# Kernel tuning notes

Hardware: AMD Instinct MI355X
Metric: run time of the kernel (lower is better)

## Reference

```python
import jax, jax.numpy as jnp
import numpy as np

B, N, IN, HID, OUT = 32, 128, 64, 128, 64
_off = np.ones((N, N)) - np.eye(N)
RECV, SEND = np.where(_off)  # rel_rec one-hot rows -> receiver idx, rel_send -> sender idx
E = N * (N - 1)


def _bn(x, g, b):
    # BatchNorm1d in training mode over flattened (B*M, C), eps=1e-5, biased var
    c = x.shape[-1]
    xf = x.reshape(-1, c)
    m = xf.mean(0)
    v = ((xf - m) ** 2).mean(0)
    return (((xf - m) / jnp.sqrt(v + 1e-5)) * g + b).reshape(x.shape)


def _mlp(x, W1, b1, W2, b2, g, b):
    h = jax.nn.silu(x @ W1 + b1)
    h = jax.nn.silu(h @ W2 + b2)
    return _bn(h, g, b)


def setup_inputs() -> dict:
    key = jax.random.key(0)
    ks = jax.random.split(key, 8)
    p = lambda k, s: jax.random.normal(k, s, dtype=jnp.float32) * 0.05
    return {
        "node_feature": jax.random.normal(ks[0], (B, N, IN), dtype=jnp.float32),
        "nodes_mask": jnp.ones((B, N), dtype=jnp.float32),
        "edges_mask": jnp.ones((B, E), dtype=jnp.float32),
        "eW1": p(ks[1], (2 * IN, HID)), "eb1": jnp.full((HID,), 0.1, jnp.float32),
        "eW2": p(ks[2], (HID, HID)), "eb2": jnp.full((HID,), 0.1, jnp.float32),
        "eg": jnp.ones((HID,), jnp.float32), "ebt": jnp.zeros((HID,), jnp.float32),
        "nW1": p(ks[3], (HID, HID)), "nb1": jnp.full((HID,), 0.1, jnp.float32),
        "nW2": p(ks[4], (HID, HID)), "nb2": jnp.full((HID,), 0.1, jnp.float32),
        "ng": jnp.ones((HID,), jnp.float32), "nbt": jnp.zeros((HID,), jnp.float32),
        "mW1": p(ks[5], (IN + HID, HID)), "mb1": jnp.full((HID,), 0.1, jnp.float32),
        "mW2": p(ks[6], (HID, OUT)), "mb2": jnp.full((OUT,), 0.1, jnp.float32),
        "mg": jnp.ones((OUT,), jnp.float32), "mbt": jnp.zeros((OUT,), jnp.float32),
        "t_nodes": 0, "t_edges": 0,
    }


def reference(node_feature, nodes_mask, edges_mask,
              eW1, eb1, eW2, eb2, eg, ebt,
              nW1, nb1, nW2, nb2, ng, nbt,
              mW1, mb1, mW2, mb2, mg, mbt,
              t_nodes, t_edges):
    # edge_model: rel_send/rel_rec one-hot matmuls == gathers
    senders = node_feature[:, SEND, :]    # [B,E,IN]
    receivers = node_feature[:, RECV, :]  # [B,E,IN]
    ef = jnp.concatenate([senders, receivers], axis=-1)  # [B,E,2*IN]
    # skip_first_edge_type=True, edge_types=2 -> only edge_nn[1], norm=1.0
    em = edges_mask[:, :, None]
    msg = _mlp(ef, eW1, eb1, eW2, eb2, eg, ebt) * em  # [B,E,HID]
    mij = msg / 1.0
    out = mij * em       # attention=False
    mij_m = mij * em
    # node_model: rel_rec.T matmul == scatter-sum over receivers, then / N
    incoming = jnp.zeros((B, N, HID), msg.dtype).at[:, RECV, :].add(out) / N
    incoming = _mlp(incoming, nW1, nb1, nW2, nb2, ng, nbt) * nodes_mask[:, :, None]
    nef = jnp.concatenate([node_feature, incoming], axis=-1)  # [B,N,IN+HID]
    out_node = _mlp(nef, mW1, mb1, mW2, mb2, mg, mbt) * nodes_mask[:, :, None]
    return (out_node, mij_m)
```

## Files before the change

kernel.cpp:

```cpp
#include <hip/hip_runtime.h>
#include <hip/hip_bf16.h>

#define BB    32
#define NNODE 128
#define INF   64
#define HIDF  128
#define OUTF  64
#define EE    (NNODE*(NNODE-1))
#define TILES 127
#define NBLK_EDGE (BB*TILES)
#define ROWS_E 520192.0f
#define ROWS_N 4096.0f
#define OUT0_ELEMS (BB*NNODE*OUTF)
#define H2_ELEMS ((size_t)520192*128)

typedef __bf16 bf16_t;
typedef __bf16 bfrag8 __attribute__((ext_vector_type(8)));
typedef float  floatx4 __attribute__((ext_vector_type(4)));

__device__ __forceinline__ float ld_g(const void* p, size_t i, int bf) {
    return bf ? (float)((const bf16_t*)p)[i] : ((const float*)p)[i];
}
__device__ __forceinline__ void st_g(void* p, size_t i, float v, int bf) {
    if (bf) ((bf16_t*)p)[i] = (bf16_t)v; else ((float*)p)[i] = v;
}
__device__ __forceinline__ void* mij_ptr(void* dout, int bf) {
    return bf ? (void*)((bf16_t*)dout + OUT0_ELEMS)
              : (void*)((float*)dout + OUT0_ELEMS);
}
__device__ __forceinline__ float silu_f(float x) {
    return x * __builtin_amdgcn_rcpf(1.0f + __expf(-x));
}

__device__ __forceinline__ int swz_col(int row, int col)  {
    return col ^ ((row & 15) << 3);
}
__device__ __forceinline__ int swz64_col(int row, int col) {
    return col ^ ((row & 7) << 3);
}

__global__ __launch_bounds__(256)
void k_prep(const unsigned int* __restrict__ eg_words,
            const void* __restrict__ W1g, const void* __restrict__ W2g,
            bf16_t* __restrict__ Wf1, bf16_t* __restrict__ Wf2,
            int* __restrict__ flag, float* __restrict__ totE)
{
    const int bf = (eg_words[0] == 0x3F803F80u) ? 1 : 0;
    if (blockIdx.x == 0) {
        if (threadIdx.x == 0) *flag = bf;
        totE[threadIdx.x] = 0.f;
    }
    const int idx = blockIdx.x*256 + threadIdx.x;
    const int mat = idx >> 14;
    const int e   = idx & 16383;
    const int n   = e & 127, k = e >> 7;
    const float v = ld_g(mat ? W2g : W1g, e, bf);
    const int NB = n >> 4, ln = n & 15;
    const int ks = k >> 5, q = (k >> 3) & 3, j = k & 7;
    bf16_t* dst = mat ? Wf2 : Wf1;
    dst[((((NB*4 + ks)*4 + q)*16 + ln) << 3) + j] = (bf16_t)v;
}

__global__ __launch_bounds__(256)
void k_sr(const void* __restrict__ nf,
          const bf16_t* __restrict__ Wf1, const void* __restrict__ b1g,
          float* __restrict__ Sbuf, float* __restrict__ Rbuf,
          const int* __restrict__ flagp)
{
    __shared__ __align__(16) bf16_t lA[128*64];
    const int bf  = *flagp;
    const int r0  = blockIdx.x * 128;
    const int tid = threadIdx.x;

#pragma unroll
    for (int s = 0; s < 4; ++s) {
        const int u = tid + s*256;
        const int m = u >> 3;
        const int c = (u & 7) ^ (m & 7);
        const size_t gi = (size_t)(r0 + m)*INF + c*8;
        if (bf) {
            ((uint4*)lA)[u] = *(const uint4*)((const bf16_t*)nf + gi);
        } else {
            const float4 f0 = *(const float4*)((const float*)nf + gi);
            const float4 f1 = *(const float4*)((const float*)nf + gi + 4);
            bfrag8 v;
            v[0]=(bf16_t)f0.x; v[1]=(bf16_t)f0.y; v[2]=(bf16_t)f0.z; v[3]=(bf16_t)f0.w;
            v[4]=(bf16_t)f1.x; v[5]=(bf16_t)f1.y; v[6]=(bf16_t)f1.z; v[7]=(bf16_t)f1.w;
            *(bfrag8*)(lA + (size_t)u*8) = v;
        }
    }
    __syncthreads();

    const int w  = tid >> 6;
    const int L  = tid & 63;
    const int wr = w >> 1;
    const int wc = w & 1;
    const int q  = L >> 4;
    const int ln = L & 15;

    const floatx4 zero4 = {0.f, 0.f, 0.f, 0.f};
    floatx4 accS[4][4], accR[4][4];
#pragma unroll
    for (int mt = 0; mt < 4; ++mt)
#pragma unroll
        for (int nt = 0; nt < 4; ++nt) { accS[mt][nt] = zero4; accR[mt][nt] = zero4; }

#pragma unroll
    for (int ks = 0; ks < 2; ++ks) {
        bfrag8 af[4], bs[4], br[4];
#pragma unroll
        for (int mt = 0; mt < 4; ++mt) {
            const int Rr = wr*64 + mt*16 + ln;
            af[mt] = *(const bfrag8*)(lA + Rr*64 + swz64_col(Rr, ks*32 + q*8));
        }
#pragma unroll
        for (int nt = 0; nt < 4; ++nt) {
            bs[nt] = *(const bfrag8*)(Wf1 + ((size_t)((wc*4 + nt)*4 + ks)*64 + L)*8);
            br[nt] = *(const bfrag8*)(Wf1 + ((size_t)((wc*4 + nt)*4 + ks + 2)*64 + L)*8);
        }
#pragma unroll
        for (int mt = 0; mt < 4; ++mt)
#pragma unroll
            for (int nt = 0; nt < 4; ++nt) {
                accS[mt][nt] = __builtin_amdgcn_mfma_f32_16x16x32_bf16(
                    af[mt], bs[nt], accS[mt][nt], 0, 0, 0);
                accR[mt][nt] = __builtin_amdgcn_mfma_f32_16x16x32_bf16(
                    af[mt], br[nt], accR[mt][nt], 0, 0, 0);
            }
    }

#pragma unroll
    for (int nt = 0; nt < 4; ++nt) {
        const int col = wc*64 + nt*16 + ln;
        const float bias = ld_g(b1g, col, bf);
#pragma unroll
        for (int mt = 0; mt < 4; ++mt)
#pragma unroll
            for (int r = 0; r < 4; ++r) {
                const int row = wr*64 + mt*16 + q*4 + r;
                Sbuf[(size_t)(r0 + row)*128 + col] = accS[mt][nt][r] + bias;
                Rbuf[(size_t)(r0 + row)*128 + col] = accR[mt][nt][r];
            }
    }
}

__global__ __launch_bounds__(256, 4)
void k_edge_mlp(const float* __restrict__ Sbuf, const float* __restrict__ Rbuf,
                const bf16_t* __restrict__ Wf2, const void* __restrict__ b2g,
                void* __restrict__ dout, bf16_t* __restrict__ h2ws,
                const int* __restrict__ flagp, float* __restrict__ totE,
                int h2mode)
{
    __shared__ __align__(16) bf16_t lA[128*128];
    __shared__ float sSum[128], sQ[128];
    const int bf  = *flagp;
    void* h2out = mij_ptr(dout, bf);
    const int bx   = blockIdx.x;
    const int bIdx = bx / TILES;
    const int t    = bx - bIdx*TILES;
    const int tid  = threadIdx.x;

    if (tid < 128) { sSum[tid] = 0.f; sQ[tid] = 0.f; }

    {
        const size_t nodeBase = (size_t)bIdx*NNODE*128;
#pragma unroll
        for (int s = 0; s < 8; ++s) {
            const int u = tid + s*256;
            const int m = u >> 4;
            const int c = (u & 15) ^ (m & 15);
            const int eb = t*128 + m;
            const unsigned recv = ((unsigned)eb * 33027u) >> 22;
            const unsigned rr   = (unsigned)eb - recv*127u;
            const unsigned send = rr + (rr >= recv ? 1u : 0u);
            const float* Sp = Sbuf + nodeBase + (size_t)send*128 + c*8;
            const float* Rp = Rbuf + nodeBase + (size_t)recv*128 + c*8;
            const float4 s0 = *(const float4*)Sp;
            const float4 s1 = *(const float4*)(Sp + 4);
            const float4 r0v = *(const float4*)Rp;
            const float4 r1v = *(const float4*)(Rp + 4);
            bfrag8 v;
            v[0]=(bf16_t)silu_f(s0.x + r0v.x); v[1]=(bf16_t)silu_f(s0.y + r0v.y);
            v[2]=(bf16_t)silu_f(s0.z + r0v.z); v[3]=(bf16_t)silu_f(s0.w + r0v.w);
            v[4]=(bf16_t)silu_f(s1.x + r1v.x); v[5]=(bf16_t)silu_f(s1.y + r1v.y);
            v[6]=(bf16_t)silu_f(s1.z + r1v.z); v[7]=(bf16_t)silu_f(s1.w + r1v.w);
            *(bfrag8*)(lA + (size_t)u*8) = v;
        }
    }
    __syncthreads();

    const int w  = tid >> 6;
    const int L  = tid & 63;
    const int wr = w >> 1;
    const int wc = w & 1;
    const int q  = L >> 4;
    const int ln = L & 15;

    const floatx4 zero4 = {0.f, 0.f, 0.f, 0.f};
    floatx4 acc[4][4];
#pragma unroll
    for (int mt = 0; mt < 4; ++mt)
#pragma unroll
        for (int nt = 0; nt < 4; ++nt) acc[mt][nt] = zero4;

#pragma unroll
    for (int ks = 0; ks < 4; ++ks) {
        const int kk = ks*32;
        bfrag8 af[4], bv[4];
#pragma unroll
        for (int mt = 0; mt < 4; ++mt) {
            const int R = wr*64 + mt*16 + ln;
            af[mt] = *(const bfrag8*)(lA + R*128 + swz_col(R, kk + q*8));
        }
#pragma unroll
        for (int nt = 0; nt < 4; ++nt)
            bv[nt] = *(const bfrag8*)(Wf2 + ((size_t)((wc*4 + nt)*4 + ks)*64 + L)*8);
#pragma unroll
        for (int mt = 0; mt < 4; ++mt)
#pragma unroll
            for (int nt = 0; nt < 4; ++nt)
                acc[mt][nt] = __builtin_amdgcn_mfma_f32_16x16x32_bf16(
                    af[mt], bv[nt], acc[mt][nt], 0, 0, 0);
    }
    __syncthreads();

#pragma unroll
    for (int nt = 0; nt < 4; ++nt) {
        const int col = wc*64 + nt*16 + ln;
        const float bias = ld_g(b2g, col, bf);
        float cs = 0.f, cq = 0.f;
#pragma unroll
        for (int mt = 0; mt < 4; ++mt)
#pragma unroll
            for (int r = 0; r < 4; ++r) {
                const int R = wr*64 + mt*16 + q*4 + r;
                const float v = silu_f(acc[mt][nt][r] + bias);
                cs += v; cq += v*v;
                lA[R*128 + swz_col(R, col)] = (bf16_t)v;
            }
        cs += __shfl_xor(cs, 16); cs += __shfl_xor(cs, 32);
        cq += __shfl_xor(cq, 16); cq += __shfl_xor(cq, 32);
        if (L < 16) { atomicAdd(&sSum[col], cs); atomicAdd(&sQ[col], cq); }
    }
    __syncthreads();

    {
        const size_t Rbase = ((size_t)bIdx*EE + (size_t)t*128) * 128;
#pragma unroll
        for (int s = 0; s < 8; ++s) {
            const int u = tid + s*256;
            const int m = u >> 4;
            const int c = (u & 15) ^ (m & 15);
            const size_t go = Rbase + (size_t)m*128 + c*8;
            if (h2mode) {
                *(uint4*)(h2ws + go) = ((const uint4*)lA)[u];
            } else if (bf) {
                *(uint4*)((bf16_t*)h2out + go) = ((const uint4*)lA)[u];
            } else {
                const bfrag8 vv = *(const bfrag8*)(lA + (size_t)u*8);
                float4 f0, f1;
                f0.x=(float)vv[0]; f0.y=(float)vv[1]; f0.z=(float)vv[2]; f0.w=(float)vv[3];
                f1.x=(float)vv[4]; f1.y=(float)vv[5]; f1.z=(float)vv[6]; f1.w=(float)vv[7];
                *(float4*)((float*)h2out + go)     = f0;
                *(float4*)((float*)h2out + go + 4) = f1;
            }
        }
        if (tid < 128) {
            atomicAdd(&totE[tid],       sSum[tid]);
            atomicAdd(&totE[128 + tid], sQ[tid]);
        }
    }
}

__global__ __launch_bounds__(256)
void k_bn_scatter(void* __restrict__ dout,
                  const bf16_t* __restrict__ h2ws,
                  const void* __restrict__ emask,
                  const float* __restrict__ totE,
                  const void* __restrict__ g, const void* __restrict__ bt,
                  float* __restrict__ inc,
                  const int* __restrict__ flagp, int h2mode)
{
    const int bf = *flagp;
    void* mij = mij_ptr(dout, bf);
    const void* h2 = h2mode ? (const void*)h2ws : (const void*)mij;
    const int h2bf = h2mode | bf;
    const int bx = blockIdx.x;
    const int b  = bx >> 7, i = bx & 127;
    const int tid = threadIdx.x;
    const int cg = tid & 15, p = tid >> 4;
    const int c0 = cg*8;
    float al[8], be[8];
#pragma unroll
    for (int j = 0; j < 8; ++j) {
        const int c = c0 + j;
        const float mn = totE[c] * (1.0f/ROWS_E);
        float vr = totE[128 + c] * (1.0f/ROWS_E) - mn*mn;
        vr = fmaxf(vr, 0.f);
        al[j] = ld_g(g, c, bf) * rsqrtf(vr + 1e-5f);
        be[j] = ld_g(bt, c, bf) - mn*al[j];
    }
    const size_t seg = (size_t)b*EE + (size_t)i*127;
    float s[8];
#pragma unroll
    for (int j = 0; j < 8; ++j) s[j] = 0.f;
    for (int e = p; e < 127; e += 16) {
        const float em  = ld_g(emask, seg + e, bf);
        const float em2 = em*em;
        const size_t base = (seg + e)*128 + c0;
        float v[8];
        if (h2bf) {
            const bfrag8 u = *(const bfrag8*)((const bf16_t*)h2 + base);
#pragma unroll
            for (int j = 0; j < 8; ++j) v[j] = (float)u[j];
        } else {
            const float4 f0 = *(const float4*)((const float*)h2 + base);
            const float4 f1 = *(const float4*)((const float*)h2 + base + 4);
            v[0]=f0.x; v[1]=f0.y; v[2]=f0.z; v[3]=f0.w;
            v[4]=f1.x; v[5]=f1.y; v[6]=f1.z; v[7]=f1.w;
        }
#pragma unroll
        for (int j = 0; j < 8; ++j) { v[j] = (v[j]*al[j] + be[j])*em2; s[j] += v[j]; }
        if (bf) {
            bfrag8 u;
#pragma unroll
            for (int j = 0; j < 8; ++j) u[j] = (bf16_t)v[j];
            *(bfrag8*)((bf16_t*)mij + base) = u;
        } else {
            float4 f0, f1;
            f0.x=v[0]; f0.y=v[1]; f0.z=v[2]; f0.w=v[3];
            f1.x=v[4]; f1.y=v[5]; f1.z=v[6]; f1.w=v[7];
            *(float4*)((float*)mij + base)     = f0;
            *(float4*)((float*)mij + base + 4) = f1;
        }
    }
    __shared__ float sm[16][128];
#pragma unroll
    for (int j = 0; j < 8; ++j) sm[p][c0+j] = s[j];
    __syncthreads();
    if (tid < 128) {
        float tsum = 0.f;
#pragma unroll
        for (int wk = 0; wk < 16; ++wk) tsum += sm[wk][tid];
        inc[(size_t)(b*NNODE + i)*HIDF + tid] = tsum * (1.0f/NNODE);
    }
}

__global__ __launch_bounds__(128)
void k_node_mlp(const float* __restrict__ inc,
                const void* __restrict__ W1g, const void* __restrict__ b1g,
                const void* __restrict__ W2g, const void* __restrict__ b2g,
                float* __restrict__ h2n, float* __restrict__ partialN,
                const int* __restrict__ flagp)
{
    const int bf = *flagp;
    __shared__ float x[16][128];
    __shared__ float h[16][128];
    const int bx = blockIdx.x;
    const int tid = threadIdx.x;
    const int r0 = bx*16;
    for (int r = 0; r < 16; ++r) x[r][tid] = inc[(size_t)(r0 + r)*128 + tid];
    __syncthreads();

    float a1[16];
#pragma unroll
    for (int r = 0; r < 16; ++r) a1[r] = 0.f;
#pragma unroll 8
    for (int k = 0; k < 128; ++k) {
        const float wv = ld_g(W1g, k*128 + tid, bf);
#pragma unroll
        for (int r = 0; r < 16; ++r) a1[r] += x[r][k]*wv;
    }
    const float bias1 = ld_g(b1g, tid, bf);
#pragma unroll
    for (int r = 0; r < 16; ++r) h[r][tid] = silu_f(a1[r] + bias1);
    __syncthreads();

    float a2[16];
#pragma unroll
    for (int r = 0; r < 16; ++r) a2[r] = 0.f;
#pragma unroll 8
    for (int k = 0; k < 128; ++k) {
        const float wv = ld_g(W2g, k*128 + tid, bf);
#pragma unroll
        for (int r = 0; r < 16; ++r) a2[r] += h[r][k]*wv;
    }
    const float bias2 = ld_g(b2g, tid, bf);
    float s = 0.f, sq = 0.f;
#pragma unroll
    for (int r = 0; r < 16; ++r) {
        const float v = silu_f(a2[r] + bias2);
        h2n[(size_t)(r0 + r)*128 + tid] = v;
        s += v; sq += v*v;
    }
    partialN[(size_t)bx*256 + tid]       = s;
    partialN[(size_t)bx*256 + 128 + tid] = sq;
}

__global__ void k_finalize_node(const float* __restrict__ p,
                                const void* __restrict__ g,
                                const void* __restrict__ bt,
                                float* __restrict__ ab,
                                const int* __restrict__ flagp)
{
    const int bf = *flagp;
    const int c = threadIdx.x;
    float s = 0.f, qv = 0.f;
#pragma unroll 8
    for (int blk = 0; blk < 256; ++blk) { s += p[blk*256 + c]; qv += p[blk*256 + 128 + c]; }
    const float m = s / ROWS_N;
    float v = qv / ROWS_N - m*m;
    v = fmaxf(v, 0.f);
    const float a = ld_g(g, c, bf) * rsqrtf(v + 1e-5f);
    ab[c]       = a;
    ab[128 + c] = ld_g(bt, c, bf) - m*a;
}

__global__ __launch_bounds__(128)
void k_final_mlp(const void* __restrict__ nf,
                 const float* __restrict__ h2n, const float* __restrict__ abn,
                 const void* __restrict__ nmask,
                 const void* __restrict__ W1g, const void* __restrict__ b1g,
                 const void* __restrict__ W2g, const void* __restrict__ b2g,
                 float* __restrict__ hm, float* __restrict__ partialM,
                 const int* __restrict__ flagp)
{
    const int bf = *flagp;
    __shared__ float x[16][192];
    __shared__ float h[16][128];
    const int bx = blockIdx.x;
    const int tid = threadIdx.x;
    const int r0 = bx*16;
    const float an = abn[tid], bn = abn[128 + tid];
    for (int r = 0; r < 16; ++r) {
        const int row = r0 + r;
        const float mask = ld_g(nmask, row, bf);
        if (tid < 64) x[r][tid] = ld_g(nf, (size_t)row*INF + tid, bf);
        x[r][64 + tid] = (h2n[(size_t)row*128 + tid]*an + bn) * mask;
    }
    __syncthreads();

    float a1[16];
#pragma unroll
    for (int r = 0; r < 16; ++r) a1[r] = 0.f;
#pragma unroll 8
    for (int k = 0; k < 192; ++k) {
        const float wv = ld_g(W1g, k*128 + tid, bf);
#pragma unroll
        for (int r = 0; r < 16; ++r) a1[r] += x[r][k]*wv;
    }
    const float bias1 = ld_g(b1g, tid, bf);
#pragma unroll
    for (int r = 0; r < 16; ++r) h[r][tid] = silu_f(a1[r] + bias1);
    __syncthreads();

    if (tid < 64) {
        float a2[16];
#pragma unroll
        for (int r = 0; r < 16; ++r) a2[r] = 0.f;
#pragma unroll 8
        for (int k = 0; k < 128; ++k) {
            const float wv = ld_g(W2g, k*64 + tid, bf);
#pragma unroll
            for (int r = 0; r < 16; ++r) a2[r] += h[r][k]*wv;
        }
        const float bias2 = ld_g(b2g, tid, bf);
        float s = 0.f, sq = 0.f;
#pragma unroll
        for (int r = 0; r < 16; ++r) {
            const float v = silu_f(a2[r] + bias2);
            hm[(size_t)(r0 + r)*OUTF + tid] = v;
            s += v; sq += v*v;
        }
        partialM[(size_t)bx*128 + tid]      = s;
        partialM[(size_t)bx*128 + 64 + tid] = sq;
    }
}

__global__ void k_finalize_m(const float* __restrict__ p,
                             const void* __restrict__ g,
                             const void* __restrict__ bt,
                             float* __restrict__ ab,
                             const int* __restrict__ flagp)
{
    const int bf = *flagp;
    const int c = threadIdx.x;
    float s = 0.f, qv = 0.f;
#pragma unroll 8
    for (int blk = 0; blk < 256; ++blk) { s += p[blk*128 + c]; qv += p[blk*128 + 64 + c]; }
    const float m = s / ROWS_N;
    float v = qv / ROWS_N - m*m;
    v = fmaxf(v, 0.f);
    const float a = ld_g(g, c, bf) * rsqrtf(v + 1e-5f);
    ab[c]      = a;
    ab[64 + c] = ld_g(bt, c, bf) - m*a;
}

__global__ void k_out_node(const float* __restrict__ hm,
                           const float* __restrict__ abm,
                           const void* __restrict__ nmask,
                           void* __restrict__ dout,
                           const int* __restrict__ flagp)
{
    const int bf = *flagp;
    const int idx = blockIdx.x*256 + threadIdx.x;
    if (idx >= OUT0_ELEMS) return;
    const int c = idx & 63;
    const int row = idx >> 6;
    const float v = (hm[idx]*abm[c] + abm[64 + c]) * ld_g(nmask, row, bf);
    st_g(dout, idx, v, bf);
}

extern "C" void kernel_launch(void* const* d_in, const int* in_sizes, int n_in,
                              void* d_out, int out_size, void* d_ws, size_t ws_size,
                              hipStream_t stream)
{
    const void* nf    = d_in[0];
    const void* nmask = d_in[1];
    const void* emask = d_in[2];
    const void* eW1   = d_in[3];
    const void* eb1   = d_in[4];
    const void* eW2   = d_in[5];
    const void* eb2   = d_in[6];
    const void* eg    = d_in[7];
    const void* ebt   = d_in[8];
    const void* nW1   = d_in[9];
    const void* nb1   = d_in[10];
    const void* nW2   = d_in[11];
    const void* nb2   = d_in[12];
    const void* ng    = d_in[13];
    const void* nbt   = d_in[14];
    const void* mW1   = d_in[15];
    const void* mb1   = d_in[16];
    const void* mW2   = d_in[17];
    const void* mb2   = d_in[18];
    const void* mg    = d_in[19];
    const void* mbt   = d_in[20];

    float* W    = (float*)d_ws;
    int*   flag = (int*)W;
    float* totE = W    + 64;
    float* abE  = totE + 256;
    float* inc  = abE  + 256;
    float* h2n  = inc  + 524288;
    float* pN   = h2n  + 524288;
    float* abN  = pN   + 65536;
    float* hm   = abN  + 256;
    float* pM   = hm   + 262144;
    float* abM  = pM   + 32768;
    bf16_t* Wf1 = (bf16_t*)(abM + 128);
    bf16_t* Wf2 = Wf1 + 16384;
    float* Sbuf = (float*)(Wf2 + 16384);
    float* Rbuf = Sbuf + 524288;
    bf16_t* h2ws = (bf16_t*)(Rbuf + 524288);

    const size_t base_bytes = (size_t)((char*)h2ws - (char*)d_ws);
    const int h2mode = (ws_size >= base_bytes + H2_ELEMS*2 + 256) ? 1 : 0;

    k_prep<<<dim3(128), dim3(256), 0, stream>>>((const unsigned int*)eg, eW1, eW2, Wf1, Wf2, flag, totE);
    k_sr<<<dim3(32), dim3(256), 0, stream>>>(nf, Wf1, eb1, Sbuf, Rbuf, flag);
    k_edge_mlp<<<dim3(NBLK_EDGE), dim3(256), 0, stream>>>(Sbuf, Rbuf, Wf2, eb2, d_out, h2ws, flag, totE, h2mode);
    k_bn_scatter<<<dim3(BB*NNODE), dim3(256), 0, stream>>>(d_out, h2ws, emask, totE, eg, ebt, inc, flag, h2mode);
    k_node_mlp<<<dim3(256), dim3(128), 0, stream>>>(inc, nW1, nb1, nW2, nb2, h2n, pN, flag);
    k_finalize_node<<<dim3(1), dim3(128), 0, stream>>>(pN, ng, nbt, abN, flag);
    k_final_mlp<<<dim3(256), dim3(128), 0, stream>>>(nf, h2n, abN, nmask, mW1, mb1, mW2, mb2, hm, pM, flag);
    k_finalize_m<<<dim3(1), dim3(64), 0, stream>>>(pM, mg, mbt, abM, flag);
    k_out_node<<<dim3(1024), dim3(256), 0, stream>>>(hm, abM, nmask, d_out, flag);
}
```

Baseline: 616.4 us.

## Transpose edge MFMA to store directly from registers and fuse BN finalize kernels

The edge MLP second GEMM now computes the transposed product (weights as A operand), so each lane holds four consecutive channels of one edge. It applies SiLU and writes the result straight to global memory, skipping the LDS round trip and two barriers. Column statistics are reduced with shuffles across lanes. The two single-block BN finalize kernels are folded into their consumer kernels, which removes two launches but makes every block redundantly reduce 256 partials. The output kernel also now handles four elements per thread.

```diff
diff --git a/kernel.cpp b/kernel.cpp
--- a/kernel.cpp
+++ b/kernel.cpp
@@ -16,6 +16,7 @@
 
 typedef __bf16 bf16_t;
 typedef __bf16 bfrag8 __attribute__((ext_vector_type(8)));
+typedef __bf16 bfrag4 __attribute__((ext_vector_type(4)));
 typedef float  floatx4 __attribute__((ext_vector_type(4)));
 
 __device__ __forceinline__ float ld_g(const void* p, size_t i, int bf) {
@@ -199,76 +200,82 @@
     const floatx4 zero4 = {0.f, 0.f, 0.f, 0.f};
     floatx4 acc[4][4];
 #pragma unroll
-    for (int mt = 0; mt < 4; ++mt)
-#pragma unroll
-        for (int nt = 0; nt < 4; ++nt) acc[mt][nt] = zero4;
+    for (int ct = 0; ct < 4; ++ct)
+#pragma unroll
+        for (int mt = 0; mt < 4; ++mt) acc[ct][mt] = zero4;
 
 #pragma unroll
     for (int ks = 0; ks < 4; ++ks) {
         const int kk = ks*32;
-        bfrag8 af[4], bv[4];
+        bfrag8 wf[4], hf[4];
+#pragma unroll
+        for (int ct = 0; ct < 4; ++ct)
+            wf[ct] = *(const bfrag8*)(Wf2 + ((size_t)((wc*4 + ct)*4 + ks)*64 + L)*8);
 #pragma unroll
         for (int mt = 0; mt < 4; ++mt) {
             const int R = wr*64 + mt*16 + ln;
-            af[mt] = *(const bfrag8*)(lA + R*128 + swz_col(R, kk + q*8));
-        }
-#pragma unroll
-        for (int nt = 0; nt < 4; ++nt)
-            bv[nt] = *(const bfrag8*)(Wf2 + ((size_t)((wc*4 + nt)*4 + ks)*64 + L)*8);
-#pragma unroll
-        for (int mt = 0; mt < 4; ++mt)
-#pragma unroll
-            for (int nt = 0; nt < 4; ++nt)
-                acc[mt][nt] = __builtin_amdgcn_mfma_f32_16x16x32_bf16(
-                    af[mt], bv[nt], acc[mt][nt], 0, 0, 0);
-    }
-    __syncthreads();
-
-#pragma unroll
-    for (int nt = 0; nt < 4; ++nt) {
-        const int col = wc*64 + nt*16 + ln;
-        const float bias = ld_g(b2g, col, bf);
-        float cs = 0.f, cq = 0.f;
-#pragma unroll
-        for (int mt = 0; mt < 4; ++mt)
-#pragma unroll
-            for (int r = 0; r < 4; ++r) {
-                const int R = wr*64 + mt*16 + q*4 + r;
-                const float v = silu_f(acc[mt][nt][r] + bias);
-                cs += v; cq += v*v;
-                lA[R*128 + swz_col(R, col)] = (bf16_t)v;
-            }
-        cs += __shfl_xor(cs, 16); cs += __shfl_xor(cs, 32);
-        cq += __shfl_xor(cq, 16); cq += __shfl_xor(cq, 32);
-        if (L < 16) { atomicAdd(&sSum[col], cs); atomicAdd(&sQ[col], cq); }
-    }
-    __syncthreads();
+            hf[mt] = *(const bfrag8*)(lA + R*128 + swz_col(R, kk + q*8));
+        }
+#pragma unroll
+        for (int ct = 0; ct < 4; ++ct)
+#pragma unroll
+            for (int mt = 0; mt < 4; ++mt)
+                acc[ct][mt] = __builtin_amdgcn_mfma_f32_16x16x32_bf16(
+                    wf[ct], hf[mt], acc[ct][mt], 0, 0, 0);
+    }
 
     {
         const size_t Rbase = ((size_t)bIdx*EE + (size_t)t*128) * 128;
 #pragma unroll
-        for (int s = 0; s < 8; ++s) {
-            const int u = tid + s*256;
-            const int m = u >> 4;
-            const int c = (u & 15) ^ (m & 15);
-            const size_t go = Rbase + (size_t)m*128 + c*8;
-            if (h2mode) {
-                *(uint4*)(h2ws + go) = ((const uint4*)lA)[u];
-            } else if (bf) {
-                *(uint4*)((bf16_t*)h2out + go) = ((const uint4*)lA)[u];
-            } else {
-                const bfrag8 vv = *(const bfrag8*)(lA + (size_t)u*8);
-                float4 f0, f1;
-                f0.x=(float)vv[0]; f0.y=(float)vv[1]; f0.z=(float)vv[2]; f0.w=(float)vv[3];
-                f1.x=(float)vv[4]; f1.y=(float)vv[5]; f1.z=(float)vv[6]; f1.w=(float)vv[7];
-                *(float4*)((float*)h2out + go)     = f0;
-                *(float4*)((float*)h2out + go + 4) = f1;
+        for (int ct = 0; ct < 4; ++ct) {
+            const int ch0 = wc*64 + ct*16 + q*4;
+            float b4[4];
+#pragma unroll
+            for (int r = 0; r < 4; ++r) b4[r] = ld_g(b2g, ch0 + r, bf);
+            float cs[4] = {0.f,0.f,0.f,0.f}, cq[4] = {0.f,0.f,0.f,0.f};
+#pragma unroll
+            for (int mt = 0; mt < 4; ++mt) {
+                const int edge = wr*64 + mt*16 + ln;
+                float v[4];
+#pragma unroll
+                for (int r = 0; r < 4; ++r) {
+                    v[r] = silu_f(acc[ct][mt][r] + b4[r]);
+                    cs[r] += v[r]; cq[r] += v[r]*v[r];
+                }
+                const size_t off = Rbase + (size_t)edge*128 + ch0;
+                if (h2mode) {
+                    bfrag4 pk;
+#pragma unroll
+                    for (int r = 0; r < 4; ++r) pk[r] = (bf16_t)v[r];
+                    *(bfrag4*)(h2ws + off) = pk;
+                } else if (bf) {
+                    bfrag4 pk;
+#pragma unroll
+                    for (int r = 0; r < 4; ++r) pk[r] = (bf16_t)v[r];
+                    *(bfrag4*)((bf16_t*)h2out + off) = pk;
+                } else {
+                    float4 f; f.x=v[0]; f.y=v[1]; f.z=v[2]; f.w=v[3];
+                    *(float4*)((float*)h2out + off) = f;
+                }
             }
-        }
-        if (tid < 128) {
-            atomicAdd(&totE[tid],       sSum[tid]);
-            atomicAdd(&totE[128 + tid], sQ[tid]);
-        }
+#pragma unroll
+            for (int r = 0; r < 4; ++r) {
+                float a = cs[r], b = cq[r];
+                a += __shfl_xor(a, 1); a += __shfl_xor(a, 2);
+                a += __shfl_xor(a, 4); a += __shfl_xor(a, 8);
+                b += __shfl_xor(b, 1); b += __shfl_xor(b, 2);
+                b += __shfl_xor(b, 4); b += __shfl_xor(b, 8);
+                if (ln == 0) {
+                    atomicAdd(&sSum[ch0 + r], a);
+                    atomicAdd(&sQ[ch0 + r], b);
+                }
+            }
+        }
+    }
+    __syncthreads();
+    if (tid < 128) {
+        atomicAdd(&totE[tid],       sSum[tid]);
+        atomicAdd(&totE[128 + tid], sQ[tid]);
     }
 }
 
@@ -397,28 +404,10 @@
     partialN[(size_t)bx*256 + 128 + tid] = sq;
 }
 
-__global__ void k_finalize_node(const float* __restrict__ p,
-                                const void* __restrict__ g,
-                                const void* __restrict__ bt,
-                                float* __restrict__ ab,
-                                const int* __restrict__ flagp)
-{
-    const int bf = *flagp;
-    const int c = threadIdx.x;
-    float s = 0.f, qv = 0.f;
-#pragma unroll 8
-    for (int blk = 0; blk < 256; ++blk) { s += p[blk*256 + c]; qv += p[blk*256 + 128 + c]; }
-    const float m = s / ROWS_N;
-    float v = qv / ROWS_N - m*m;
-    v = fmaxf(v, 0.f);
-    const float a = ld_g(g, c, bf) * rsqrtf(v + 1e-5f);
-    ab[c]       = a;
-    ab[128 + c] = ld_g(bt, c, bf) - m*a;
-}
-
 __global__ __launch_bounds__(128)
 void k_final_mlp(const void* __restrict__ nf,
-                 const float* __restrict__ h2n, const float* __restrict__ abn,
+                 const float* __restrict__ h2n, const float* __restrict__ pN,
+                 const void* __restrict__ ng, const void* __restrict__ nbt,
                  const void* __restrict__ nmask,
                  const void* __restrict__ W1g, const void* __restrict__ b1g,
                  const void* __restrict__ W2g, const void* __restrict__ b2g,
@@ -431,7 +420,16 @@
     const int bx = blockIdx.x;
     const int tid = threadIdx.x;
     const int r0 = bx*16;
-    const float an = abn[tid], bn = abn[128 + tid];
+
+    float sB = 0.f, qB = 0.f;
+#pragma unroll 8
+    for (int blk = 0; blk < 256; ++blk) { sB += pN[blk*256 + tid]; qB += pN[blk*256 + 128 + tid]; }
+    const float mnN = sB / ROWS_N;
+    float vrN = qB / ROWS_N - mnN*mnN;
+    vrN = fmaxf(vrN, 0.f);
+    const float an = ld_g(ng, tid, bf) * rsqrtf(vrN + 1e-5f);
+    const float bn = ld_g(nbt, tid, bf) - mnN*an;
+
     for (int r = 0; r < 16; ++r) {
         const int row = r0 + r;
         const float mask = ld_g(nmask, row, bf);
@@ -477,38 +475,37 @@
     }
 }
 
-__global__ void k_finalize_m(const float* __restrict__ p,
-                             const void* __restrict__ g,
-                             const void* __restrict__ bt,
-                             float* __restrict__ ab,
-                             const int* __restrict__ flagp)
+__global__ __launch_bounds__(256)
+void k_out_node(const float* __restrict__ hm,
+                const float* __restrict__ pM,
+                const void* __restrict__ mg, const void* __restrict__ mbt,
+                const void* __restrict__ nmask,
+                void* __restrict__ dout,
+                const int* __restrict__ flagp)
 {
     const int bf = *flagp;
-    const int c = threadIdx.x;
-    float s = 0.f, qv = 0.f;
+    const int tid = threadIdx.x;
+    __shared__ float sab[128];
+    if (tid < 64) {
+        float s = 0.f, qv = 0.f;
 #pragma unroll 8
-    for (int blk = 0; blk < 256; ++blk) { s += p[blk*128 + c]; qv += p[blk*128 + 64 + c]; }
-    const float m = s / ROWS_N;
-    float v = qv / ROWS_N - m*m;
-    v = fmaxf(v, 0.f);
-    const float a = ld_g(g, c, bf) * rsqrtf(v + 1e-5f);
-    ab[c]      = a;
-    ab[64 + c] = ld_g(bt, c, bf) - m*a;
-}
-
-__global__ void k_out_node(const float* __restrict__ hm,
-                           const float* __restrict__ abm,
-                           const void* __restrict__ nmask,
-                           void* __restrict__ dout,
-                           const int* __restrict__ flagp)
-{
-    const int bf = *flagp;
-    const int idx = blockIdx.x*256 + threadIdx.x;
-    if (idx >= OUT0_ELEMS) return;
-    const int c = idx & 63;
-    const int row = idx >> 6;
-    const float v = (hm[idx]*abm[c] + abm[64 + c]) * ld_g(nmask, row, bf);
-    st_g(dout, idx, v, bf);
+        for (int blk = 0; blk < 256; ++blk) { s += pM[blk*128 + tid]; qv += pM[blk*128 + 64 + tid]; }
+        const float mn = s / ROWS_N;
+        float vr = qv / ROWS_N - mn*mn;
+        vr = fmaxf(vr, 0.f);
+        const float a = ld_g(mg, tid, bf) * rsqrtf(vr + 1e-5f);
+        sab[tid]      = a;
+        sab[64 + tid] = ld_g(mbt, tid, bf) - mn*a;
+    }
+    __syncthreads();
+#pragma unroll
+    for (int s = 0; s < 4; ++s) {
+        const int idx = blockIdx.x*1024 + s*256 + tid;
+        const int c = idx & 63;
+        const int row = idx >> 6;
+        const float v = (hm[idx]*sab[c] + sab[64 + c]) * ld_g(nmask, row, bf);
+        st_g(dout, idx, v, bf);
+    }
 }
 
 extern "C" void kernel_launch(void* const* d_in, const int* in_sizes, int n_in,
@@ -562,8 +559,6 @@
     k_edge_mlp<<<dim3(NBLK_EDGE), dim3(256), 0, stream>>>(Sbuf, Rbuf, Wf2, eb2, d_out, h2ws, flag, totE, h2mode);
     k_bn_scatter<<<dim3(BB*NNODE), dim3(256), 0, stream>>>(d_out, h2ws, emask, totE, eg, ebt, inc, flag, h2mode);
     k_node_mlp<<<dim3(256), dim3(128), 0, stream>>>(inc, nW1, nb1, nW2, nb2, h2n, pN, flag);
-    k_finalize_node<<<dim3(1), dim3(128), 0, stream>>>(pN, ng, nbt, abN, flag);
-    k_final_mlp<<<dim3(256), dim3(128), 0, stream>>>(nf, h2n, abN, nmask, mW1, mb1, mW2, mb2, hm, pM, flag);
-    k_finalize_m<<<dim3(1), dim3(64), 0, stream>>>(pM, mg, mbt, abM, flag);
-    k_out_node<<<dim3(1024), dim3(256), 0, stream>>>(hm, abM, nmask, d_out, flag);
-}
+    k_final_mlp<<<dim3(256), dim3(128), 0, stream>>>(nf, h2n, pN, ng, nbt, nmask, mW1, mb1, mW2, mb2, hm, pM, flag);
+    k_out_node<<<dim3(256), dim3(256), 0, stream>>>(hm, pM, mg, mbt, nmask, d_out, flag);
+}
```

Result: slower. 640.6 us (+3.9%).
